# Kernel tuning notes

Hardware: AMD Instinct MI355X
Metric: run time of the kernel (lower is better)

## Reference

```python
import jax, jax.numpy as jnp
import numpy as np

N, E, DIM = 50000, 1_600_000, 96
H = DIM // 3      # num_heads = dim/3 = 32
HD = 3            # head_dim = dim/num_heads = 3
SCALE = 2.0
EPS = 1e-5


def ln(x, g, b):
    mu = x.mean(-1, keepdims=True)
    var = ((x - mu) ** 2).mean(-1, keepdims=True)
    return (x - mu) * jax.lax.rsqrt(var + EPS) * g + b


def setup_inputs() -> dict:
    key = jax.random.key(0)
    ks = jax.random.split(key, 40)
    rn = lambda k, shp, s=0.05: jax.random.normal(k, shp, jnp.float32) * s
    inp = {
        'feat': jax.random.normal(ks[0], (N, DIM), jnp.float32),
        'edge': jax.random.normal(ks[1], (E, H), jnp.float32),
        'Wq': rn(ks[2], (DIM, DIM)), 'bq': jnp.zeros((DIM,), jnp.float32),
        'Wk': rn(ks[3], (DIM, DIM)), 'bk': jnp.zeros((DIM,), jnp.float32),
        'Wv': rn(ks[4], (DIM, DIM)), 'bv': jnp.zeros((DIM,), jnp.float32),
        'We': rn(ks[5], (H, H)), 'be': jnp.zeros((H,), jnp.float32),
        'Wb': rn(ks[6], (H, H)), 'bb': jnp.zeros((H,), jnp.float32),
        'Wvv': rn(ks[7], (DIM + H, DIM)), 'bvv': jnp.zeros((DIM,), jnp.float32),
        'Wf0': rn(ks[8], (H, 2 * H)), 'bf0': jnp.zeros((2 * H,), jnp.float32),
        'Wf1': rn(ks[9], (2 * H, H)), 'bf1': jnp.zeros((H,), jnp.float32),
        'Wm0': rn(ks[10], (DIM, 2 * DIM)), 'bm0': jnp.zeros((2 * DIM,), jnp.float32),
        'Wm1': rn(ks[11], (2 * DIM, DIM)), 'bm1': jnp.zeros((DIM,), jnp.float32),
        'g_n0': jnp.ones((DIM,), jnp.float32), 'b_n0': jnp.zeros((DIM,), jnp.float32),
        'g_e0': jnp.ones((H,), jnp.float32), 'b_e0': jnp.zeros((H,), jnp.float32),
        'g_e1': jnp.ones((H,), jnp.float32), 'b_e1': jnp.zeros((H,), jnp.float32),
        'g_m': jnp.ones((DIM,), jnp.float32), 'b_m': jnp.zeros((DIM,), jnp.float32),
        'w': jnp.zeros((1,), jnp.float32),
        'src': jax.random.randint(ks[12], (E,), 0, N),
        'dst': jax.random.randint(ks[13], (E,), 0, N),
    }
    return inp


def reference(feat, edge, Wq, bq, Wk, bk, Wv, bv, We, be, Wb, bb, Wvv, bvv,
              Wf0, bf0, Wf1, bf1, Wm0, bm0, Wm1, bm1,
              g_n0, b_n0, g_e0, b_e0, g_e1, b_e1, g_m, b_m, w, src, dst):
    n = feat.shape[0]
    h0 = ln(feat, g_n0, b_n0)            # [N, DIM]
    ew = ln(edge, g_e0, b_e0)            # [E, H]
    q = (h0 @ Wq + bq).reshape(n, H, HD)
    k = (h0 @ Wk + bk).reshape(n, H, HD)
    v = (h0 @ Wv + bv).reshape(n, H, HD)
    ve = (ew @ We + be)[:, :, None]       # [E, H, 1]
    B = ew @ Wb + bb                      # [E, H]
    # src_dot_dst('k','q'): (k[src] * q[dst]).sum(-1)
    score = jnp.sum(k[src] * q[dst], axis=-1) / SCALE + B   # [E, H]
    e = score + edge                       # [E, H]
    se = jnp.concatenate([v[src], ve], axis=-1)              # [E, H, 4]
    # edge_softmax: softmax over incoming edges of each dst node, per head
    m = jax.ops.segment_max(score, dst, num_segments=n)      # [N, H]
    ex = jnp.exp(score - m[dst])
    den = jax.ops.segment_sum(ex, dst, num_segments=n)
    att = (ex / den[dst])[:, :, None]                        # [E, H, 1]
    agg = jax.ops.segment_sum(att * se, dst, num_segments=n) # [N, H, 4]
    h = feat * (1.0 + w) + (agg.reshape(n, -1) @ Wvv + bvv)  # [N, DIM]
    # up_expert Mlp (pre-LN residual)
    hn = ln(h, g_m, b_m)
    h = h + (jax.nn.relu(hn @ Wm0 + bm0) @ Wm1 + bm1)
    # edge FFN residual
    en = ln(e, g_e1, b_e1)
    e = e + (jax.nn.relu(en @ Wf0 + bf0) @ Wf1 + bf1)
    return h, e
```

## Files before the change

kernel.cpp:

```cpp
#include <hip/hip_runtime.h>
#include <cstdint>
#include <cstddef>


typedef short  s16x8 __attribute__((ext_vector_type(8)));
typedef float  f32x4 __attribute__((ext_vector_type(4)));

__device__ __forceinline__ unsigned short f2b(float x) {
    union { float f; unsigned u; } v; v.f = x;
    unsigned r = v.u + 0x7FFF + ((v.u >> 16) & 1);
    return (unsigned short)(r >> 16);
}
__device__ __forceinline__ float b2f(unsigned short u) {
    union { unsigned u; float f; } v; v.u = ((unsigned)u) << 16; return v.f;
}

__device__ __forceinline__ float red32(float v) {
    #pragma unroll
    for (int m = 16; m >= 1; m >>= 1) v += __shfl_xor(v, m, 64);
    return v;
}

__global__ __launch_bounds__(256) void ln96_kernel(
    const float* __restrict__ x, const float* __restrict__ g,
    const float* __restrict__ b, float* __restrict__ y, int M)
{
    int lane = threadIdx.x & 31;
    int grp  = threadIdx.x >> 5;
    int r = blockIdx.x * 8 + grp;
    if (r >= M) return;
    const float* xr = x + (size_t)r * 96;
    float a0 = xr[lane], a1 = xr[lane + 32], a2 = xr[lane + 64];
    float mu = red32(a0 + a1 + a2) * (1.f / 96.f);
    float d0 = a0 - mu, d1 = a1 - mu, d2 = a2 - mu;
    float var = red32(d0 * d0 + d1 * d1 + d2 * d2) * (1.f / 96.f);
    float rs = rsqrtf(var + 1e-5f);
    float* yr = y + (size_t)r * 96;
    yr[lane]      = d0 * rs * g[lane]      + b[lane];
    yr[lane + 32] = d1 * rs * g[lane + 32] + b[lane + 32];
    yr[lane + 64] = d2 * rs * g[lane + 64] + b[lane + 64];
}

template<int MULTI, int RELU, int RES>
__global__ __launch_bounds__(256) void mgemm_kernel(
    const float* __restrict__ A, int lda,
    const float* __restrict__ B0, const float* __restrict__ B1,
    const float* __restrict__ B2, int ldb,
    const float* __restrict__ bias0, const float* __restrict__ bias1,
    const float* __restrict__ bias2,
    const float* __restrict__ resid,
    const float* __restrict__ wptr,
    float* __restrict__ C, int ldc,
    unsigned short* __restrict__ C16,
    int M, int K)
{
    __shared__ unsigned short sA[64 * 40];
    __shared__ unsigned short sB[96 * 40];

    const int tid = threadIdx.x;
    const int m0 = blockIdx.x * 64;
    const int y  = blockIdx.y;
    const float* B = MULTI ? (y == 0 ? B0 : (y == 1 ? B1 : B2)) : B0;
    const int nbB = MULTI ? 0 : y * 96;
    const int nbC = y * 96;

    const int w = tid >> 6, l = tid & 63, fr = l & 15, kg = l >> 4;

    f32x4 acc[6];
    #pragma unroll
    for (int i = 0; i < 6; i++) acc[i] = (f32x4){0.f, 0.f, 0.f, 0.f};

    for (int kc = 0; kc < K; kc += 32) {
        {
            int row = tid >> 2, k8 = (tid & 3) * 8;
            int grow = m0 + row;
            s16x8 a8 = {0, 0, 0, 0, 0, 0, 0, 0};
            if (grow < M) {
                float4 v0 = *(const float4*)(A + (size_t)grow * lda + kc + k8);
                float4 v1 = *(const float4*)(A + (size_t)grow * lda + kc + k8 + 4);
                a8[0] = (short)f2b(v0.x); a8[1] = (short)f2b(v0.y);
                a8[2] = (short)f2b(v0.z); a8[3] = (short)f2b(v0.w);
                a8[4] = (short)f2b(v1.x); a8[5] = (short)f2b(v1.y);
                a8[6] = (short)f2b(v1.z); a8[7] = (short)f2b(v1.w);
            }
            *(s16x8*)&sA[row * 40 + k8] = a8;
        }
        #pragma unroll
        for (int r = 0; r < 3; r++) {
            int idx = tid + 256 * r;
            int k = idx / 24;
            int n4 = (idx - k * 24) * 4;
            float4 v = *(const float4*)(B + (size_t)(kc + k) * ldb + nbB + n4);
            sB[(n4 + 0) * 40 + k] = f2b(v.x);
            sB[(n4 + 1) * 40 + k] = f2b(v.y);
            sB[(n4 + 2) * 40 + k] = f2b(v.z);
            sB[(n4 + 3) * 40 + k] = f2b(v.w);
        }
        __syncthreads();
        {
            s16x8 a = *(s16x8*)&sA[(16 * w + fr) * 40 + kg * 8];
            #pragma unroll
            for (int nt = 0; nt < 6; nt++) {
                s16x8 b = *(s16x8*)&sB[(16 * nt + fr) * 40 + kg * 8];
                acc[nt] = __builtin_amdgcn_mfma_f32_16x16x32_bf16(a, b, acc[nt], 0, 0, 0);
            }
        }
        __syncthreads();
    }

    float scale = 1.f;
    if (RES) scale = wptr ? (1.f + wptr[0]) : 1.f;
    const float* biasp = MULTI ? (y == 0 ? bias0 : (y == 1 ? bias1 : bias2)) : bias0;
    const int bbase = MULTI ? 0 : nbB;

    #pragma unroll
    for (int nt = 0; nt < 6; nt++) {
        int cl = nt * 16 + fr;
        float bv = biasp[bbase + cl];
        int gcol = nbC + cl;
        #pragma unroll
        for (int r = 0; r < 4; r++) {
            int row = m0 + 16 * w + 4 * kg + r;
            if (row >= M) continue;
            float v = acc[nt][r] + bv;
            if (RELU) v = fmaxf(v, 0.f);
            if (RES) v += scale * resid[(size_t)row * ldc + gcol];
            C[(size_t)row * ldc + gcol] = v;
            if (MULTI && C16 != nullptr && y == 2)
                C16[(size_t)row * 96 + cl] = f2b(v);
        }
    }
}

__global__ __launch_bounds__(256) void count_kernel(
    const int* __restrict__ dst, int* __restrict__ cnt, int E)
{
    int i = blockIdx.x * 256 + threadIdx.x;
    if (i < E) atomicAdd(&cnt[dst[i]], 1);
}

__global__ __launch_bounds__(1024) void scan_kernel(
    const int* __restrict__ cnt, int* __restrict__ off, int* __restrict__ cur, int N)
{
    __shared__ int s[1024];
    const int tid = threadIdx.x;
    const int chunk = (N + 1023) >> 10;
    const int lo = tid * chunk;
    const int hi = min(lo + chunk, N);
    int sum = 0;
    for (int i = lo; i < hi; i++) sum += cnt[i];
    s[tid] = sum;
    __syncthreads();
    for (int d = 1; d < 1024; d <<= 1) {
        int v = (tid >= d) ? s[tid - d] : 0;
        __syncthreads();
        s[tid] += v;
        __syncthreads();
    }
    int base = (tid == 0) ? 0 : s[tid - 1];
    for (int i = lo; i < hi; i++) {
        off[i] = base; cur[i] = base;
        base += cnt[i];
    }
}

__global__ __launch_bounds__(256) void scatter_kernel(
    const int* __restrict__ dst, const int* __restrict__ src,
    int* __restrict__ cur, int* __restrict__ pos, int* __restrict__ srcs, int E)
{
    int i = blockIdx.x * 256 + threadIdx.x;
    if (i < E) {
        int p = atomicAdd(&cur[dst[i]], 1);
        pos[i] = p;
        srcs[p] = src[i];
    }
}

__global__ __launch_bounds__(256, 4) void edge_tile_kernel(
    const float* __restrict__ edge, const float* __restrict__ qkv,
    const int* __restrict__ src, const int* __restrict__ dst,
    const int* __restrict__ pos,
    const float* __restrict__ We, const float* __restrict__ be,
    const float* __restrict__ Wb, const float* __restrict__ bb,
    const float* __restrict__ Wf0, const float* __restrict__ bf0,
    const float* __restrict__ Wf1, const float* __restrict__ bf1,
    const float* __restrict__ ge0, const float* __restrict__ be0,
    const float* __restrict__ ge1, const float* __restrict__ be1,
    unsigned short* __restrict__ exve16, float* __restrict__ eout, int E)
{
    __shared__ float          sEV[64 * 36];
    __shared__ unsigned short sQK[64 * 40];
    __shared__ unsigned short sA [64 * 40];
    __shared__ unsigned short sB [64 * 40];
    __shared__ unsigned short sB2[32 * 72];
    __shared__ unsigned short sX [64 * 72];

    const int tid = threadIdx.x;
    const long long e0 = (long long)blockIdx.x * 64;
    const int w  = tid >> 6;
    const int l  = tid & 63;
    const int fr = l & 15;
    const int kg = l >> 4;

    {
        const int row = tid >> 2;
        const int j   = tid & 3;
        long long e = e0 + row;
        float q[24], k[24];
        if (e < E) {
            int dn = dst[e], sn = src[e];
            const float* qp = qkv + (size_t)dn * 288 + 24 * j;
            const float* kp = qkv + (size_t)sn * 288 + 96 + 24 * j;
            #pragma unroll
            for (int t = 0; t < 6; t++) {
                *(float4*)&q[t * 4] = *(const float4*)(qp + t * 4);
                *(float4*)&k[t * 4] = *(const float4*)(kp + t * 4);
            }
        } else {
            #pragma unroll
            for (int t = 0; t < 24; t++) { q[t] = 0.f; k[t] = 0.f; }
        }
        s16x8 qkb;
        #pragma unroll
        for (int t = 0; t < 8; t++) {
            float d = k[3*t]*q[3*t] + k[3*t+1]*q[3*t+1] + k[3*t+2]*q[3*t+2];
            qkb[t] = (short)f2b(0.5f * d);
        }
        *(s16x8*)&sQK[row * 40 + 8 * j] = qkb;
    }

    #pragma unroll
    for (int rr = 0; rr < 2; rr++) {
        int idx = tid + 256 * rr;
        int row = idx >> 3, c4 = (idx & 7) * 4;
        long long e = e0 + row;
        float4 v = make_float4(0.f, 0.f, 0.f, 0.f);
        if (e < E) v = *(const float4*)(edge + e * 32 + c4);
        *(float4*)&sEV[row * 36 + c4] = v;
    }
    {
        int k = tid >> 3, c4 = (tid & 7) * 4;
        float4 vb = *(const float4*)(Wb + k * 32 + c4);
        float4 ve = *(const float4*)(We + k * 32 + c4);
        sB[(c4 + 0) * 40 + k] = f2b(vb.x); sB[(c4 + 1) * 40 + k] = f2b(vb.y);
        sB[(c4 + 2) * 40 + k] = f2b(vb.z); sB[(c4 + 3) * 40 + k] = f2b(vb.w);
        sB[(32 + c4 + 0) * 40 + k] = f2b(ve.x); sB[(32 + c4 + 1) * 40 + k] = f2b(ve.y);
        sB[(32 + c4 + 2) * 40 + k] = f2b(ve.z); sB[(32 + c4 + 3) * 40 + k] = f2b(ve.w);
    }
    #pragma unroll
    for (int rr = 0; rr < 2; rr++) {
        int idx = tid + 256 * rr;
        int k = idx >> 3, c4 = (idx & 7) * 4;
        float4 v = *(const float4*)(Wf1 + k * 32 + c4);
        sB2[(c4 + 0) * 72 + k] = f2b(v.x); sB2[(c4 + 1) * 72 + k] = f2b(v.y);
        sB2[(c4 + 2) * 72 + k] = f2b(v.z); sB2[(c4 + 3) * 72 + k] = f2b(v.w);
    }
    __syncthreads();

    {
        const int row = 16 * w + (tid & 15);
        const int q = (tid & 63) >> 4;
        float x[8];
        *(float4*)&x[0] = *(float4*)&sEV[row * 36 + 8 * q];
        *(float4*)&x[4] = *(float4*)&sEV[row * 36 + 8 * q + 4];
        float s = x[0] + x[1] + x[2] + x[3] + x[4] + x[5] + x[6] + x[7];
        s += __shfl_xor(s, 16, 64); s += __shfl_xor(s, 32, 64);
        float mu = s * (1.f / 32.f);
        float v2 = 0.f;
        #pragma unroll
        for (int i = 0; i < 8; i++) { float d = x[i] - mu; v2 += d * d; }
        v2 += __shfl_xor(v2, 16, 64); v2 += __shfl_xor(v2, 32, 64);
        float rs = rsqrtf(v2 * (1.f / 32.f) + 1e-5f);
        float4 g1 = *(const float4*)(ge0 + 8 * q), g2 = *(const float4*)(ge0 + 8 * q + 4);
        float4 b1 = *(const float4*)(be0 + 8 * q), b2 = *(const float4*)(be0 + 8 * q + 4);
        float gg[8] = {g1.x, g1.y, g1.z, g1.w, g2.x, g2.y, g2.z, g2.w};
        float bs[8] = {b1.x, b1.y, b1.z, b1.w, b2.x, b2.y, b2.z, b2.w};
        s16x8 y;
        #pragma unroll
        for (int i = 0; i < 8; i++)
            y[i] = (short)f2b((x[i] - mu) * rs * gg[i] + bs[i]);
        *(s16x8*)&sA[row * 40 + 8 * q] = y;
    }
    __syncthreads();

    f32x4 acc[4];
    {
        s16x8 a = *(s16x8*)&sA[(16 * w + fr) * 40 + kg * 8];
        #pragma unroll
        for (int nt = 0; nt < 4; nt++) {
            s16x8 b = *(s16x8*)&sB[(16 * nt + fr) * 40 + kg * 8];
            f32x4 z = {0.f, 0.f, 0.f, 0.f};
            acc[nt] = __builtin_amdgcn_mfma_f32_16x16x32_bf16(a, b, z, 0, 0, 0);
        }
    }
    __syncthreads();

    #pragma unroll
    for (int nt = 0; nt < 2; nt++) {
        int col = nt * 16 + fr;
        float bbv = bb[col];
        #pragma unroll
        for (int r = 0; r < 4; r++) {
            int row = 16 * w + 4 * kg + r;
            float sc = acc[nt][r] + b2f(sQK[row * 40 + col]) + bbv;
            sX[row * 72 + col] = f2b(__expf(sc));
            float er = sc + sEV[row * 36 + col];
            sEV[row * 36 + col] = er;
        }
    }
    #pragma unroll
    for (int nt = 2; nt < 4; nt++) {
        int col = (nt - 2) * 16 + fr;
        float bev = be[col];
        #pragma unroll
        for (int r = 0; r < 4; r++) {
            int row = 16 * w + 4 * kg + r;
            sX[row * 72 + 32 + col] = f2b(acc[nt][r] + bev);
        }
    }
    #pragma unroll
    for (int rr = 0; rr < 2; rr++) {
        int idx = tid + 256 * rr;
        int k = idx >> 4, c4 = (idx & 15) * 4;
        float4 v = *(const float4*)(Wf0 + k * 64 + c4);
        sB[(c4 + 0) * 40 + k] = f2b(v.x); sB[(c4 + 1) * 40 + k] = f2b(v.y);
        sB[(c4 + 2) * 40 + k] = f2b(v.z); sB[(c4 + 3) * 40 + k] = f2b(v.w);
    }
    __syncthreads();

    #pragma unroll
    for (int rr = 0; rr < 2; rr++) {
        int idx = tid + 256 * rr;
        int row = idx >> 3, c8 = (idx & 7) * 8;
        long long e = e0 + row;
        if (e < E) {
            int p = pos[e];
            *(s16x8*)(exve16 + (size_t)p * 64 + c8) = *(s16x8*)&sX[row * 72 + c8];
        }
    }
    {
        const int row = 16 * w + (tid & 15);
        const int q = (tid & 63) >> 4;
        float x[8];
        *(float4*)&x[0] = *(float4*)&sEV[row * 36 + 8 * q];
        *(float4*)&x[4] = *(float4*)&sEV[row * 36 + 8 * q + 4];
        float s = x[0] + x[1] + x[2] + x[3] + x[4] + x[5] + x[6] + x[7];
        s += __shfl_xor(s, 16, 64); s += __shfl_xor(s, 32, 64);
        float mu = s * (1.f / 32.f);
        float v2 = 0.f;
        #pragma unroll
        for (int i = 0; i < 8; i++) { float d = x[i] - mu; v2 += d * d; }
        v2 += __shfl_xor(v2, 16, 64); v2 += __shfl_xor(v2, 32, 64);
        float rs = rsqrtf(v2 * (1.f / 32.f) + 1e-5f);
        float4 g1 = *(const float4*)(ge1 + 8 * q), g2 = *(const float4*)(ge1 + 8 * q + 4);
        float4 b1 = *(const float4*)(be1 + 8 * q), b2 = *(const float4*)(be1 + 8 * q + 4);
        float gg[8] = {g1.x, g1.y, g1.z, g1.w, g2.x, g2.y, g2.z, g2.w};
        float bs[8] = {b1.x, b1.y, b1.z, b1.w, b2.x, b2.y, b2.z, b2.w};
        s16x8 y;
        #pragma unroll
        for (int i = 0; i < 8; i++)
            y[i] = (short)f2b((x[i] - mu) * rs * gg[i] + bs[i]);
        *(s16x8*)&sA[row * 40 + 8 * q] = y;
    }
    __syncthreads();

    {
        s16x8 a = *(s16x8*)&sA[(16 * w + fr) * 40 + kg * 8];
        #pragma unroll
        for (int nt = 0; nt < 4; nt++) {
            s16x8 b = *(s16x8*)&sB[(16 * nt + fr) * 40 + kg * 8];
            f32x4 z = {0.f, 0.f, 0.f, 0.f};
            f32x4 a2 = __builtin_amdgcn_mfma_f32_16x16x32_bf16(a, b, z, 0, 0, 0);
            int col = nt * 16 + fr;
            float b0v = bf0[col];
            #pragma unroll
            for (int r = 0; r < 4; r++) {
                int row = 16 * w + 4 * kg + r;
                sX[row * 72 + col] = f2b(fmaxf(a2[r] + b0v, 0.f));
            }
        }
    }
    __syncthreads();

    {
        s16x8 a0 = *(s16x8*)&sX[(16 * w + fr) * 72 + kg * 8];
        s16x8 a1 = *(s16x8*)&sX[(16 * w + fr) * 72 + 32 + kg * 8];
        #pragma unroll
        for (int nt = 0; nt < 2; nt++) {
            s16x8 b0 = *(s16x8*)&sB2[(16 * nt + fr) * 72 + kg * 8];
            s16x8 b1 = *(s16x8*)&sB2[(16 * nt + fr) * 72 + 32 + kg * 8];
            f32x4 z = {0.f, 0.f, 0.f, 0.f};
            f32x4 t = __builtin_amdgcn_mfma_f32_16x16x32_bf16(a0, b0, z, 0, 0, 0);
            t = __builtin_amdgcn_mfma_f32_16x16x32_bf16(a1, b1, t, 0, 0, 0);
            int col = nt * 16 + fr;
            float bf1v = bf1[col];
            #pragma unroll
            for (int r = 0; r < 4; r++) {
                int row = 16 * w + 4 * kg + r;
                float out = t[r] + sEV[row * 36 + col] + bf1v;
                sEV[row * 36 + col] = out;
            }
        }
    }
    __syncthreads();

    #pragma unroll
    for (int rr = 0; rr < 2; rr++) {
        int idx = tid + 256 * rr;
        int row = idx >> 3, c4 = (idx & 7) * 4;
        long long e = e0 + row;
        if (e < E)
            *(float4*)(eout + e * 32 + c4) = *(float4*)&sEV[row * 36 + c4];
    }
}

__global__ __launch_bounds__(256) void gather_kernel(
    const unsigned short* __restrict__ exve16, const unsigned short* __restrict__ v16,
    const int* __restrict__ srcs, const int* __restrict__ off,
    const int* __restrict__ cnt, float* __restrict__ agg, int N)
{
    __shared__ unsigned short sV16[4][2][96];
    __shared__ unsigned short sE16[4][2][64];
    const int wave = threadIdx.x >> 6;
    const int lane = threadIdx.x & 63;
    const int head = lane & 31;
    const int half = lane >> 5;
    int n = blockIdx.x * 4 + wave;
    if (n >= N) return;
    const int o = off[n], d = cnt[n];
    float a0 = 0.f, a1 = 0.f, a2 = 0.f, a3 = 0.f, den = 0.f;
    for (int i = half; i < d; i += 2) {
        int sn = srcs[o + i];
        const unsigned short* vr = v16 + (size_t)sn * 96;
        const unsigned short* er = exve16 + (size_t)(o + i) * 64;
        if (head < 12) {
            *(s16x8*)&sV16[wave][half][head * 8] = *(const s16x8*)(vr + head * 8);
        } else if (head >= 24) {
            int j = head - 24;
            *(s16x8*)&sE16[wave][half][j * 8] = *(const s16x8*)(er + j * 8);
        }
        __builtin_amdgcn_wave_barrier();
        float ex = b2f(sE16[wave][half][head]);
        float vv = b2f(sE16[wave][half][32 + head]);
        a0 += ex * b2f(sV16[wave][half][head * 3]);
        a1 += ex * b2f(sV16[wave][half][head * 3 + 1]);
        a2 += ex * b2f(sV16[wave][half][head * 3 + 2]);
        a3 += ex * vv;
        den += ex;
        __builtin_amdgcn_wave_barrier();
    }
    a0 += __shfl_xor(a0, 32, 64);
    a1 += __shfl_xor(a1, 32, 64);
    a2 += __shfl_xor(a2, 32, 64);
    a3 += __shfl_xor(a3, 32, 64);
    den += __shfl_xor(den, 32, 64);
    if (half == 0) {
        float sc = (d > 0) ? 1.f / den : 0.f;
        float* ap = agg + (size_t)n * 128 + head * 4;
        ap[0] = a0 * sc; ap[1] = a1 * sc; ap[2] = a2 * sc; ap[3] = a3 * sc;
    }
}

extern "C" void kernel_launch(void* const* d_in, const int* in_sizes, int n_in,
                              void* d_out, int out_size, void* d_ws, size_t ws_size,
                              hipStream_t stream)
{
    (void)n_in; (void)out_size; (void)ws_size;
    const float* feat = (const float*)d_in[0];
    const float* edge = (const float*)d_in[1];
    const float* Wq   = (const float*)d_in[2];
    const float* bq   = (const float*)d_in[3];
    const float* Wk   = (const float*)d_in[4];
    const float* bk   = (const float*)d_in[5];
    const float* Wv   = (const float*)d_in[6];
    const float* bv   = (const float*)d_in[7];
    const float* We   = (const float*)d_in[8];
    const float* be   = (const float*)d_in[9];
    const float* Wb   = (const float*)d_in[10];
    const float* bb   = (const float*)d_in[11];
    const float* Wvv  = (const float*)d_in[12];
    const float* bvv  = (const float*)d_in[13];
    const float* Wf0  = (const float*)d_in[14];
    const float* bf0  = (const float*)d_in[15];
    const float* Wf1  = (const float*)d_in[16];
    const float* bf1  = (const float*)d_in[17];
    const float* Wm0  = (const float*)d_in[18];
    const float* bm0  = (const float*)d_in[19];
    const float* Wm1  = (const float*)d_in[20];
    const float* bm1  = (const float*)d_in[21];
    const float* g_n0 = (const float*)d_in[22];
    const float* b_n0 = (const float*)d_in[23];
    const float* g_e0 = (const float*)d_in[24];
    const float* b_e0 = (const float*)d_in[25];
    const float* g_e1 = (const float*)d_in[26];
    const float* b_e1 = (const float*)d_in[27];
    const float* g_m  = (const float*)d_in[28];
    const float* b_m  = (const float*)d_in[29];
    const float* wsc  = (const float*)d_in[30];
    const int*   src  = (const int*)d_in[31];
    const int*   dst  = (const int*)d_in[32];

    const int N = in_sizes[0] / 96;
    const int E = in_sizes[1] / 32;

    float* ws    = (float*)d_ws;
    float* qkv   = ws;
    float* agg   = qkv + (size_t)N * 288;
    float* h0    = agg + (size_t)N * 128;
    float* hp    = h0 + (size_t)N * 96;
    unsigned short* v16 = (unsigned short*)(hp + (size_t)N * 96);
    unsigned short* exve16 = v16 + (size_t)N * 96;
    int*   pos   = (int*)(exve16 + (size_t)E * 64);
    int*   srcs  = pos + E;
    int*   cnt   = srcs + E;
    int*   offv  = cnt + N;
    int*   cur   = offv + N;
    float* tbuf  = ws;
    float* hout  = (float*)d_out;
    float* eoutp = (float*)d_out + (size_t)N * 96;

    hipMemsetAsync(cnt, 0, (size_t)N * sizeof(int), stream);

    const int mt = (N + 63) / 64;
    const int et = (E + 255) / 256;

    count_kernel<<<et, 256, 0, stream>>>(dst, cnt, E);
    scan_kernel<<<1, 1024, 0, stream>>>(cnt, offv, cur, N);
    scatter_kernel<<<et, 256, 0, stream>>>(dst, src, cur, pos, srcs, E);

    ln96_kernel<<<(N + 7) / 8, 256, 0, stream>>>(feat, g_n0, b_n0, h0, N);
    mgemm_kernel<1,0,0><<<dim3(mt, 3), 256, 0, stream>>>(
        h0, 96, Wq, Wk, Wv, 96, bq, bk, bv, nullptr, nullptr,
        qkv, 288, v16, N, 96);

    edge_tile_kernel<<<(E + 63) / 64, 256, 0, stream>>>(edge, qkv, src, dst, pos,
                                             We, be, Wb, bb, Wf0, bf0, Wf1, bf1,
                                             g_e0, b_e0, g_e1, b_e1,
                                             exve16, eoutp, E);

    gather_kernel<<<(N + 3) / 4, 256, 0, stream>>>(exve16, v16, srcs, offv, cnt, agg, N);

    mgemm_kernel<0,0,1><<<dim3(mt, 1), 256, 0, stream>>>(
        agg, 128, Wvv, Wvv, Wvv, 96, bvv, bvv, bvv, feat, wsc,
        hp, 96, nullptr, N, 128);
    ln96_kernel<<<(N + 7) / 8, 256, 0, stream>>>(hp, g_m, b_m, h0, N);
    mgemm_kernel<0,1,0><<<dim3(mt, 2), 256, 0, stream>>>(
        h0, 96, Wm0, Wm0, Wm0, 192, bm0, bm0, bm0, nullptr, nullptr,
        tbuf, 192, nullptr, N, 96);
    mgemm_kernel<0,0,1><<<dim3(mt, 1), 256, 0, stream>>>(
        tbuf, 192, Wm1, Wm1, Wm1, 96, bm1, bm1, bm1, hp, nullptr,
        hout, 96, nullptr, N, 192);
}
```

Before: 949.6 us.

## Fuse layernorms into GEMM A-loads, store agg as bf16, unroll gather by two

Removes the two standalone LayerNorm kernels by computing row LayerNorm inside the GEMM prologue. The whole normalized A tile is staged into a larger shared buffer once, instead of being reloaded per K chunk. The gather kernel now handles two edges per half-wave per iteration to raise memory-level parallelism, and writes the aggregate in bf16 so the following GEMM reads half the bytes. The larger shared buffer (64x200 bf16) may lower occupancy, and the node-side kernels are small next to the edge kernel.

```diff
diff --git a/kernel.cpp b/kernel.cpp
--- a/kernel.cpp
+++ b/kernel.cpp
@@ -4,6 +4,7 @@
 
 
 typedef short  s16x8 __attribute__((ext_vector_type(8)));
+typedef short  s16x4 __attribute__((ext_vector_type(4)));
 typedef float  f32x4 __attribute__((ext_vector_type(4)));
 
 __device__ __forceinline__ unsigned short f2b(float x) {
@@ -15,46 +16,19 @@
     union { unsigned u; float f; } v; v.u = ((unsigned)u) << 16; return v.f;
 }
 
-__device__ __forceinline__ float red32(float v) {
-    #pragma unroll
-    for (int m = 16; m >= 1; m >>= 1) v += __shfl_xor(v, m, 64);
-    return v;
-}
-
-__global__ __launch_bounds__(256) void ln96_kernel(
-    const float* __restrict__ x, const float* __restrict__ g,
-    const float* __restrict__ b, float* __restrict__ y, int M)
-{
-    int lane = threadIdx.x & 31;
-    int grp  = threadIdx.x >> 5;
-    int r = blockIdx.x * 8 + grp;
-    if (r >= M) return;
-    const float* xr = x + (size_t)r * 96;
-    float a0 = xr[lane], a1 = xr[lane + 32], a2 = xr[lane + 64];
-    float mu = red32(a0 + a1 + a2) * (1.f / 96.f);
-    float d0 = a0 - mu, d1 = a1 - mu, d2 = a2 - mu;
-    float var = red32(d0 * d0 + d1 * d1 + d2 * d2) * (1.f / 96.f);
-    float rs = rsqrtf(var + 1e-5f);
-    float* yr = y + (size_t)r * 96;
-    yr[lane]      = d0 * rs * g[lane]      + b[lane];
-    yr[lane + 32] = d1 * rs * g[lane + 32] + b[lane + 32];
-    yr[lane + 64] = d2 * rs * g[lane + 64] + b[lane + 64];
-}
-
-template<int MULTI, int RELU, int RES>
+template<int MULTI, int LNA, int A16, int RELU, int RES>
 __global__ __launch_bounds__(256) void mgemm_kernel(
-    const float* __restrict__ A, int lda,
+    const void* __restrict__ Av, int lda,
     const float* __restrict__ B0, const float* __restrict__ B1,
     const float* __restrict__ B2, int ldb,
     const float* __restrict__ bias0, const float* __restrict__ bias1,
     const float* __restrict__ bias2,
-    const float* __restrict__ resid,
-    const float* __restrict__ wptr,
-    float* __restrict__ C, int ldc,
-    unsigned short* __restrict__ C16,
+    const float* __restrict__ lng, const float* __restrict__ lnbv,
+    const float* __restrict__ resid, const float* __restrict__ wptr,
+    float* __restrict__ C, int ldc, unsigned short* __restrict__ C16,
     int M, int K)
 {
-    __shared__ unsigned short sA[64 * 40];
+    __shared__ unsigned short sAL[64 * 200];
     __shared__ unsigned short sB[96 * 40];
 
     const int tid = threadIdx.x;
@@ -63,33 +37,74 @@
     const float* B = MULTI ? (y == 0 ? B0 : (y == 1 ? B1 : B2)) : B0;
     const int nbB = MULTI ? 0 : y * 96;
     const int nbC = y * 96;
-
     const int w = tid >> 6, l = tid & 63, fr = l & 15, kg = l >> 4;
+    const int KP = K + 8;
+
+    if (LNA) {
+        const float* Af = (const float*)Av;
+        const int row = 16 * w + fr;
+        const int grow = m0 + row;
+        float x[24];
+        if (grow < M) {
+            #pragma unroll
+            for (int t = 0; t < 6; t++)
+                *(float4*)&x[t * 4] = *(const float4*)(Af + (size_t)grow * lda + 24 * kg + t * 4);
+        } else {
+            #pragma unroll
+            for (int t = 0; t < 24; t++) x[t] = 0.f;
+        }
+        float s = 0.f;
+        #pragma unroll
+        for (int t = 0; t < 24; t++) s += x[t];
+        s += __shfl_xor(s, 16, 64); s += __shfl_xor(s, 32, 64);
+        float mu = s * (1.f / 96.f);
+        float v2 = 0.f;
+        #pragma unroll
+        for (int t = 0; t < 24; t++) { float d = x[t] - mu; v2 += d * d; }
+        v2 += __shfl_xor(v2, 16, 64); v2 += __shfl_xor(v2, 32, 64);
+        float rs = rsqrtf(v2 * (1.f / 96.f) + 1e-5f);
+        #pragma unroll
+        for (int t3 = 0; t3 < 3; t3++) {
+            s16x8 yv;
+            #pragma unroll
+            for (int u = 0; u < 8; u++) {
+                int cidx = 24 * kg + t3 * 8 + u;
+                yv[u] = (short)f2b((x[t3 * 8 + u] - mu) * rs * lng[cidx] + lnbv[cidx]);
+            }
+            *(s16x8*)&sAL[row * KP + 24 * kg + t3 * 8] = yv;
+        }
+    } else {
+        const int nseg = K >> 3;
+        for (int idx = tid; idx < 64 * nseg; idx += 256) {
+            int row = idx / nseg, k8 = (idx - row * nseg) * 8;
+            int grow = m0 + row;
+            s16x8 a8 = (s16x8){0, 0, 0, 0, 0, 0, 0, 0};
+            if (grow < M) {
+                if (A16) {
+                    a8 = *(const s16x8*)((const unsigned short*)Av + (size_t)grow * lda + k8);
+                } else {
+                    const float* Af = (const float*)Av;
+                    float4 v0 = *(const float4*)(Af + (size_t)grow * lda + k8);
+                    float4 v1 = *(const float4*)(Af + (size_t)grow * lda + k8 + 4);
+                    a8[0] = (short)f2b(v0.x); a8[1] = (short)f2b(v0.y);
+                    a8[2] = (short)f2b(v0.z); a8[3] = (short)f2b(v0.w);
+                    a8[4] = (short)f2b(v1.x); a8[5] = (short)f2b(v1.y);
+                    a8[6] = (short)f2b(v1.z); a8[7] = (short)f2b(v1.w);
+                }
+            }
+            *(s16x8*)&sAL[row * KP + k8] = a8;
+        }
+    }
 
     f32x4 acc[6];
     #pragma unroll
     for (int i = 0; i < 6; i++) acc[i] = (f32x4){0.f, 0.f, 0.f, 0.f};
 
     for (int kc = 0; kc < K; kc += 32) {
-        {
-            int row = tid >> 2, k8 = (tid & 3) * 8;
-            int grow = m0 + row;
-            s16x8 a8 = {0, 0, 0, 0, 0, 0, 0, 0};
-            if (grow < M) {
-                float4 v0 = *(const float4*)(A + (size_t)grow * lda + kc + k8);
-                float4 v1 = *(const float4*)(A + (size_t)grow * lda + kc + k8 + 4);
-                a8[0] = (short)f2b(v0.x); a8[1] = (short)f2b(v0.y);
-                a8[2] = (short)f2b(v0.z); a8[3] = (short)f2b(v0.w);
-                a8[4] = (short)f2b(v1.x); a8[5] = (short)f2b(v1.y);
-                a8[6] = (short)f2b(v1.z); a8[7] = (short)f2b(v1.w);
-            }
-            *(s16x8*)&sA[row * 40 + k8] = a8;
-        }
         #pragma unroll
         for (int r = 0; r < 3; r++) {
             int idx = tid + 256 * r;
-            int k = idx / 24;
-            int n4 = (idx - k * 24) * 4;
+            int k = idx / 24, n4 = (idx - k * 24) * 4;
             float4 v = *(const float4*)(B + (size_t)(kc + k) * ldb + nbB + n4);
             sB[(n4 + 0) * 40 + k] = f2b(v.x);
             sB[(n4 + 1) * 40 + k] = f2b(v.y);
@@ -98,7 +113,7 @@
         }
         __syncthreads();
         {
-            s16x8 a = *(s16x8*)&sA[(16 * w + fr) * 40 + kg * 8];
+            s16x8 a = *(s16x8*)&sAL[(16 * w + fr) * KP + kc + kg * 8];
             #pragma unroll
             for (int nt = 0; nt < 6; nt++) {
                 s16x8 b = *(s16x8*)&sB[(16 * nt + fr) * 40 + kg * 8];
@@ -417,10 +432,10 @@
 __global__ __launch_bounds__(256) void gather_kernel(
     const unsigned short* __restrict__ exve16, const unsigned short* __restrict__ v16,
     const int* __restrict__ srcs, const int* __restrict__ off,
-    const int* __restrict__ cnt, float* __restrict__ agg, int N)
-{
-    __shared__ unsigned short sV16[4][2][96];
-    __shared__ unsigned short sE16[4][2][64];
+    const int* __restrict__ cnt, unsigned short* __restrict__ agg16, int N)
+{
+    __shared__ unsigned short sV16[4][2][2][96];
+    __shared__ unsigned short sE16[4][2][2][64];
     const int wave = threadIdx.x >> 6;
     const int lane = threadIdx.x & 63;
     const int head = lane & 31;
@@ -429,24 +444,45 @@
     if (n >= N) return;
     const int o = off[n], d = cnt[n];
     float a0 = 0.f, a1 = 0.f, a2 = 0.f, a3 = 0.f, den = 0.f;
-    for (int i = half; i < d; i += 2) {
-        int sn = srcs[o + i];
-        const unsigned short* vr = v16 + (size_t)sn * 96;
-        const unsigned short* er = exve16 + (size_t)(o + i) * 64;
-        if (head < 12) {
-            *(s16x8*)&sV16[wave][half][head * 8] = *(const s16x8*)(vr + head * 8);
-        } else if (head >= 24) {
-            int j = head - 24;
-            *(s16x8*)&sE16[wave][half][j * 8] = *(const s16x8*)(er + j * 8);
+    for (int i = half; i < d; i += 4) {
+        const int i2 = i + 2;
+        {
+            int sn = srcs[o + i];
+            const unsigned short* vr = v16 + (size_t)sn * 96;
+            const unsigned short* er = exve16 + (size_t)(o + i) * 64;
+            if (head < 12)
+                *(s16x8*)&sV16[wave][half][0][head * 8] = *(const s16x8*)(vr + head * 8);
+            else if (head >= 24)
+                *(s16x8*)&sE16[wave][half][0][(head - 24) * 8] = *(const s16x8*)(er + (head - 24) * 8);
+        }
+        if (i2 < d) {
+            int sn = srcs[o + i2];
+            const unsigned short* vr = v16 + (size_t)sn * 96;
+            const unsigned short* er = exve16 + (size_t)(o + i2) * 64;
+            if (head < 12)
+                *(s16x8*)&sV16[wave][half][1][head * 8] = *(const s16x8*)(vr + head * 8);
+            else if (head >= 24)
+                *(s16x8*)&sE16[wave][half][1][(head - 24) * 8] = *(const s16x8*)(er + (head - 24) * 8);
         }
         __builtin_amdgcn_wave_barrier();
-        float ex = b2f(sE16[wave][half][head]);
-        float vv = b2f(sE16[wave][half][32 + head]);
-        a0 += ex * b2f(sV16[wave][half][head * 3]);
-        a1 += ex * b2f(sV16[wave][half][head * 3 + 1]);
-        a2 += ex * b2f(sV16[wave][half][head * 3 + 2]);
-        a3 += ex * vv;
-        den += ex;
+        {
+            float ex = b2f(sE16[wave][half][0][head]);
+            float vv = b2f(sE16[wave][half][0][32 + head]);
+            a0 += ex * b2f(sV16[wave][half][0][head * 3]);
+            a1 += ex * b2f(sV16[wave][half][0][head * 3 + 1]);
+            a2 += ex * b2f(sV16[wave][half][0][head * 3 + 2]);
+            a3 += ex * vv;
+            den += ex;
+        }
+        if (i2 < d) {
+            float ex = b2f(sE16[wave][half][1][head]);
+            float vv = b2f(sE16[wave][half][1][32 + head]);
+            a0 += ex * b2f(sV16[wave][half][1][head * 3]);
+            a1 += ex * b2f(sV16[wave][half][1][head * 3 + 1]);
+            a2 += ex * b2f(sV16[wave][half][1][head * 3 + 2]);
+            a3 += ex * vv;
+            den += ex;
+        }
         __builtin_amdgcn_wave_barrier();
     }
     a0 += __shfl_xor(a0, 32, 64);
@@ -456,8 +492,12 @@
     den += __shfl_xor(den, 32, 64);
     if (half == 0) {
         float sc = (d > 0) ? 1.f / den : 0.f;
-        float* ap = agg + (size_t)n * 128 + head * 4;
-        ap[0] = a0 * sc; ap[1] = a1 * sc; ap[2] = a2 * sc; ap[3] = a3 * sc;
+        s16x4 ov;
+        ov[0] = (short)f2b(a0 * sc);
+        ov[1] = (short)f2b(a1 * sc);
+        ov[2] = (short)f2b(a2 * sc);
+        ov[3] = (short)f2b(a3 * sc);
+        *(s16x4*)(agg16 + (size_t)n * 128 + head * 4) = ov;
     }
 }
 
@@ -505,10 +545,9 @@
 
     float* ws    = (float*)d_ws;
     float* qkv   = ws;
-    float* agg   = qkv + (size_t)N * 288;
-    float* h0    = agg + (size_t)N * 128;
-    float* hp    = h0 + (size_t)N * 96;
-    unsigned short* v16 = (unsigned short*)(hp + (size_t)N * 96);
+    float* hp    = qkv + (size_t)N * 288;
+    unsigned short* agg16 = (unsigned short*)(hp + (size_t)N * 96);
+    unsigned short* v16   = agg16 + (size_t)N * 128;
     unsigned short* exve16 = v16 + (size_t)N * 96;
     int*   pos   = (int*)(exve16 + (size_t)E * 64);
     int*   srcs  = pos + E;
@@ -528,26 +567,24 @@
     scan_kernel<<<1, 1024, 0, stream>>>(cnt, offv, cur, N);
     scatter_kernel<<<et, 256, 0, stream>>>(dst, src, cur, pos, srcs, E);
 
-    ln96_kernel<<<(N + 7) / 8, 256, 0, stream>>>(feat, g_n0, b_n0, h0, N);
-    mgemm_kernel<1,0,0><<<dim3(mt, 3), 256, 0, stream>>>(
-        h0, 96, Wq, Wk, Wv, 96, bq, bk, bv, nullptr, nullptr,
-        qkv, 288, v16, N, 96);
+    mgemm_kernel<1,1,0,0,0><<<dim3(mt, 3), 256, 0, stream>>>(
+        feat, 96, Wq, Wk, Wv, 96, bq, bk, bv, g_n0, b_n0,
+        nullptr, nullptr, qkv, 288, v16, N, 96);
 
     edge_tile_kernel<<<(E + 63) / 64, 256, 0, stream>>>(edge, qkv, src, dst, pos,
                                              We, be, Wb, bb, Wf0, bf0, Wf1, bf1,
                                              g_e0, b_e0, g_e1, b_e1,
                                              exve16, eoutp, E);
 
-    gather_kernel<<<(N + 3) / 4, 256, 0, stream>>>(exve16, v16, srcs, offv, cnt, agg, N);
-
-    mgemm_kernel<0,0,1><<<dim3(mt, 1), 256, 0, stream>>>(
-        agg, 128, Wvv, Wvv, Wvv, 96, bvv, bvv, bvv, feat, wsc,
-        hp, 96, nullptr, N, 128);
-    ln96_kernel<<<(N + 7) / 8, 256, 0, stream>>>(hp, g_m, b_m, h0, N);
-    mgemm_kernel<0,1,0><<<dim3(mt, 2), 256, 0, stream>>>(
-        h0, 96, Wm0, Wm0, Wm0, 192, bm0, bm0, bm0, nullptr, nullptr,
-        tbuf, 192, nullptr, N, 96);
-    mgemm_kernel<0,0,1><<<dim3(mt, 1), 256, 0, stream>>>(
-        tbuf, 192, Wm1, Wm1, Wm1, 96, bm1, bm1, bm1, hp, nullptr,
-        hout, 96, nullptr, N, 192);
-}
+    gather_kernel<<<(N + 3) / 4, 256, 0, stream>>>(exve16, v16, srcs, offv, cnt, agg16, N);
+
+    mgemm_kernel<0,0,1,0,1><<<dim3(mt, 1), 256, 0, stream>>>(
+        agg16, 128, Wvv, Wvv, Wvv, 96, bvv, bvv, bvv, nullptr, nullptr,
+        feat, wsc, hp, 96, nullptr, N, 128);
+    mgemm_kernel<0,1,0,1,0><<<dim3(mt, 2), 256, 0, stream>>>(
+        hp, 96, Wm0, Wm0, Wm0, 192, bm0, bm0, bm0, g_m, b_m,
+        nullptr, nullptr, tbuf, 192, nullptr, N, 96);
+    mgemm_kernel<0,0,0,0,1><<<dim3(mt, 1), 256, 0, stream>>>(
+        tbuf, 192, Wm1, Wm1, Wm1, 96, bm1, bm1, bm1, nullptr, nullptr,
+        hp, nullptr, hout, 96, nullptr, N, 192);
+}
```

Result: no change. 941.5 us (-0.8%).
